# Kernel tuning notes

Hardware: AMD Instinct MI355X
Metric: run time of the kernel (lower is better)

The kernel has to match this reference:

```python
import jax, jax.numpy as jnp
import numpy as np

NA = 3          # anchors per head
NC = 3          # classes (labels < 3 are valid)
IGNORE_THRES = 0.5
OBJ_SCALE = 5.0
NOOBJ_SCALE = 0.5
GRIDS = [19, 38, 76]
SCALED_ANCHORS = [
    jnp.array([[116., 90.], [156., 198.], [373., 326.]], jnp.float32) / 32.0,  # large head
    jnp.array([[30., 61.], [62., 45.], [59., 119.]], jnp.float32) / 16.0,      # medium head
    jnp.array([[10., 13.], [16., 30.], [33., 23.]], jnp.float32) / 8.0,        # small head
]


def _safe_log(p):
    # torch BCELoss clamps log terms at -100
    return jnp.maximum(jnp.log(p), -100.0)


def _bce(p, t):
    return -(t * _safe_log(p) + (1.0 - t) * _safe_log(1.0 - p))


def _scale_loss(yolo_out, boxes, labels, anchors, G):
    B = yolo_out.shape[0]
    out = yolo_out.reshape(B, NA, G, G, -1)            # [B,3,G,G,8]
    aw = anchors[:, 0].reshape(1, NA, 1, 1)
    ah = anchors[:, 1].reshape(1, NA, 1, 1)
    # _change_bbox
    px = out[..., 0] - jnp.floor(out[..., 0])
    py = out[..., 1] - jnp.floor(out[..., 1])
    pw = jnp.log(out[..., 2] / aw + 1e-16)
    ph = jnp.log(out[..., 3] / ah + 1e-16)
    pconf = out[..., 4]
    pcls = out[..., 5:]                                 # [B,3,G,G,NC]
    # _yolo_targets (vectorized; boxes occupy distinct grid cells by construction)
    tb = boxes * G                                      # [B,nb,4]
    valid = labels < NC                                 # [B,nb]
    vf = valid.astype(out.dtype)
    gi = jnp.clip(tb[..., 0].astype(jnp.int32), 0, G - 1)
    gj = jnp.clip(tb[..., 1].astype(jnp.int32), 0, G - 1)
    bw, bh = tb[..., 2], tb[..., 3]                     # [B,nb]
    # anchor-wh IoU (same formula incl. 1e-16 placement as source)
    inter = jnp.minimum(anchors[:, 0], bw[..., None]) * jnp.minimum(anchors[:, 1], bh[..., None])
    union = anchors[:, 0] * anchors[:, 1] + 1e-16 + (bw * bh)[..., None] - inter
    iou = inter / union                                 # [B,nb,NA]
    best = jnp.argmax(iou, axis=-1)                     # [B,nb]
    bidx = jnp.arange(B)[:, None]                       # [B,1] -> broadcasts with [B,nb]
    obj = jnp.zeros((B, NA, G, G), out.dtype).at[bidx, best, gj, gi].max(vf)
    is_best = best[..., None] == jnp.arange(NA)         # [B,nb,NA]
    clear = valid[..., None] & ((iou > IGNORE_THRES) | is_best)
    keep = 1.0 - clear.astype(out.dtype)
    noobj = jnp.ones((B, NA, G, G), out.dtype).at[
        bidx[..., None], jnp.arange(NA), gj[..., None], gi[..., None]].min(keep)
    # tx/ty in the source are t_x - t_x.float() == 0, so targets stay zero
    twv = vf * jnp.log(bw / anchors[best, 0] + 1e-16)
    thv = vf * jnp.log(bh / anchors[best, 1] + 1e-16)
    tw = jnp.zeros((B, NA, G, G), out.dtype).at[bidx, best, gj, gi].set(twv)
    th = jnp.zeros((B, NA, G, G), out.dtype).at[bidx, best, gj, gi].set(thv)
    tcls = jnp.zeros((B, NA, G, G, NC), out.dtype).at[
        bidx, best, gj, gi, jnp.clip(labels, 0, NC - 1)].max(vf)
    tconf = obj
    # masked sum losses (reduction='sum' over masked elements)
    x_loss = jnp.sum(obj * px ** 2)
    y_loss = jnp.sum(obj * py ** 2)
    w_loss = jnp.sum(obj * (pw - tw) ** 2)
    h_loss = jnp.sum(obj * (ph - th) ** 2)
    conf_obj = jnp.sum(obj * _bce(pconf, tconf))
    conf_noobj = jnp.sum(noobj * _bce(pconf, tconf))
    cls_loss = jnp.sum(obj[..., None] * _bce(pcls, tcls))
    return (x_loss + y_loss + w_loss + h_loss
            + OBJ_SCALE * conf_obj + NOOBJ_SCALE * conf_noobj + cls_loss)


def reference(out_large, out_medium, out_small, boxes, labels):
    B = out_large.shape[0]
    loss = 0.0
    for out, anc, g in zip((out_large, out_medium, out_small), SCALED_ANCHORS, GRIDS):
        loss = loss + _scale_loss(out, boxes, labels, anc, g)
    return loss / B


def setup_inputs() -> dict:
    key = jax.random.key(0)
    ks = jax.random.split(key, 8)
    B, NB = 128, 12
    # predictions in (0.02, 0.98): valid BCE probs and positive w/h
    def u(k, shape):
        return 0.02 + 0.96 * jax.random.uniform(k, shape, jnp.float32)
    out_large = u(ks[0], (B, 3 * 19 * 19, 8))
    out_medium = u(ks[1], (B, 3 * 38 * 38, 8))
    out_small = u(ks[2], (B, 3 * 76 * 76, 8))
    # box centers: distinct grid columns per box at all grid sizes
    base_x = (jnp.arange(NB, dtype=jnp.float32) + 0.5) / NB
    xc = base_x[None, :] + jax.random.uniform(ks[3], (B, NB), jnp.float32, -0.004, 0.004)
    yc = jax.random.uniform(ks[4], (B, NB), jnp.float32, 0.1, 0.9)
    wh = jax.random.uniform(ks[5], (B, NB, 2), jnp.float32, 0.05, 0.4)
    boxes = jnp.concatenate([xc[..., None], yc[..., None], wh], axis=-1)
    labels = jax.random.randint(ks[6], (B, NB), 0, 5, jnp.int32)  # labels>=3 invalid
    return {"out_large": out_large, "out_medium": out_medium, "out_small": out_small,
            "boxes": boxes, "labels": labels}
```

## Files before the change

kernel.cpp:

```cpp
#include <hip/hip_runtime.h>

#define NA 3
#define NCLS 3
#define NB 12
#define BATCH 128

__device__ __forceinline__ float safelog(float x) {
    return fmaxf(logf(x), -100.0f);
}

__device__ __constant__ float AWc[3][3] = {{3.625f, 4.875f, 11.65625f},
                                           {1.875f, 3.875f, 3.6875f},
                                           {1.25f,  2.0f,   4.125f}};
__device__ __constant__ float AHc[3][3] = {{2.8125f, 6.1875f, 10.1875f},
                                           {3.8125f, 2.8125f, 7.4375f},
                                           {1.625f,  3.75f,   2.875f}};


template <int G, int S, int ITER>
__device__ __forceinline__ void scale_body(int b, int chunk,
                                           const float* __restrict__ outp,
                                           const float* __restrict__ boxes,
                                           const int* __restrict__ labels,
                                           int* sbox, float* red,
                                           float* __restrict__ partials, int pidx) {
    constexpr int CELLS = NA * G * G;
    const int tid = threadIdx.x;

    if (tid < NB) {
        float4 bx = ((const float4*)boxes)[b * NB + tid];
        int lab = labels[b * NB + tid];
        bool valid = lab < NCLS;

        float bw = bx.z * (float)G, bh = bx.w * (float)G;
        int gi = min(max((int)(bx.x * (float)G), 0), G - 1);
        int gj = min(max((int)(bx.y * (float)G), 0), G - 1);

        float iou[3]; int best = 0; float bi = -1.0f;
#pragma unroll
        for (int a = 0; a < 3; a++) {
            float aw = AWc[S][a], ah = AHc[S][a];
            float inter = fminf(aw, bw) * fminf(ah, bh);
            float uni = aw * ah + 1e-16f + bw * bh - inter;
            iou[a] = inter / uni;
            if (iou[a] > bi) { bi = iou[a]; best = a; }
        }
        int flags = 0;
        if (valid) {
#pragma unroll
            for (int a = 0; a < 3; a++)
                if (iou[a] > 0.5f || a == best) flags |= (1 << a);
            flags |= (1 << (4 + best));
        }
        sbox[tid * 6 + 0] = gi;
        sbox[tid * 6 + 1] = gj;
        sbox[tid * 6 + 2] = flags;
        sbox[tid * 6 + 3] = min(max(lab, 0), NCLS - 1);
        sbox[tid * 6 + 4] = __float_as_int(valid ? logf(bw / AWc[S][best] + 1e-16f) : 0.0f);
        sbox[tid * 6 + 5] = __float_as_int(valid ? logf(bh / AHc[S][best] + 1e-16f) : 0.0f);
    }
    __syncthreads();

    const float* outb = outp + (size_t)b * CELLS * 8;
    float acc = 0.0f;
    const int base = chunk * (256 * ITER);

#pragma unroll
    for (int k = 0; k < ITER; k++) {
        int c = base + k * 256 + tid;
        if (c < CELLS) {
            int a   = c / (G * G);
            int rem = c - a * (G * G);
            int gj  = rem / G;
            int gi  = rem - gj * G;

            const float4* p = (const float4*)(outb + (size_t)c * 8);
            float4 q0 = p[0];
            float4 q1 = p[1];

            float keepv = 1.0f;
            bool obj = false;
            float tw = 0.0f, th = 0.0f;
            int cls = 0;
#pragma unroll
            for (int n = 0; n < NB; n++) {
                if (sbox[n * 6 + 0] == gi && sbox[n * 6 + 1] == gj) {
                    int fl = sbox[n * 6 + 2];
                    if ((fl >> a) & 1) keepv = 0.0f;
                    if ((fl >> (4 + a)) & 1) {
                        obj = true;
                        cls = sbox[n * 6 + 3];
                        tw  = __int_as_float(sbox[n * 6 + 4]);
                        th  = __int_as_float(sbox[n * 6 + 5]);
                    }
                }
            }

            float conf = q1.x;
            float loss = -0.5f * keepv * safelog(1.0f - conf);

            if (obj) {
                float aw = AWc[S][a], ah = AHc[S][a];
                float px = q0.x - floorf(q0.x);
                float py = q0.y - floorf(q0.y);
                float pw = logf(q0.z / aw + 1e-16f);
                float ph = logf(q0.w / ah + 1e-16f);
                float dw = pw - tw, dh = ph - th;
                loss += px * px + py * py + dw * dw + dh * dh;
                loss += -5.0f * safelog(conf);
                float c0 = q1.y, c1 = q1.z, c2 = q1.w;
                loss -= (cls == 0) ? safelog(c0) : safelog(1.0f - c0);
                loss -= (cls == 1) ? safelog(c1) : safelog(1.0f - c1);
                loss -= (cls == 2) ? safelog(c2) : safelog(1.0f - c2);
            }
            acc += loss;
        }
    }

    red[tid] = acc;
    __syncthreads();
    for (int s = 128; s > 0; s >>= 1) {
        if (tid < s) red[tid] += red[tid + s];
        __syncthreads();
    }
    if (tid == 0) partials[pidx] = red[0];
}

__launch_bounds__(256)
__global__ void fused_loss(const float* __restrict__ oL,
                           const float* __restrict__ oM,
                           const float* __restrict__ oS,
                           const float* __restrict__ boxes,
                           const int* __restrict__ labels,
                           float* __restrict__ partials) {
    __shared__ int sbox[NB * 6];
    __shared__ float red[256];
    int idx = blockIdx.x;
    if (idx < 128) {
        scale_body<19, 0, 5>(idx, 0, oL, boxes, labels, sbox, red, partials, idx);
    } else if (idx < 640) {
        int r = idx - 128;
        scale_body<38, 1, 5>(r >> 2, r & 3, oM, boxes, labels, sbox, red, partials, idx);
    } else {
        int r = idx - 640;
        scale_body<76, 2, 8>(r / 9, r % 9, oS, boxes, labels, sbox, red, partials, idx);
    }
}

__global__ void final_reduce(const float* __restrict__ partials, int n,
                             float* __restrict__ out) {
    __shared__ float red[256];
    float acc = 0.0f;
    for (int i = threadIdx.x; i < n; i += 256) acc += partials[i];
    red[threadIdx.x] = acc;
    __syncthreads();
    for (int s = 128; s > 0; s >>= 1) {
        if (threadIdx.x < s) red[threadIdx.x] += red[threadIdx.x + s];
        __syncthreads();
    }
    if (threadIdx.x == 0) out[0] = red[0] * (1.0f / (float)BATCH);
}

extern "C" void kernel_launch(void* const* d_in, const int* in_sizes, int n_in,
                              void* d_out, int out_size, void* d_ws, size_t ws_size,
                              hipStream_t stream) {
    const float* oL     = (const float*)d_in[0];
    const float* oM     = (const float*)d_in[1];
    const float* oS     = (const float*)d_in[2];
    const float* boxes  = (const float*)d_in[3];
    const int*   labels = (const int*)d_in[4];

    float* partials = (float*)d_ws;

    fused_loss<<<1792, 256, 0, stream>>>(oL, oM, oS, boxes, labels, partials);
    final_reduce<<<1, 256, 0, stream>>>(partials, 1792, (float*)d_out);
}
```

Before: 25.83 us.

## Fuse final reduction via last-block atomic, skip box matching per wavefront, use fast log

Replaces the separate final_reduce launch with a last-block-done pattern: each block writes its partial, bumps an atomic counter, and the last block reduces all partials. A memset launch resets the counter. The per-cell loop over 12 boxes now runs only when a wavefront's cell range could hold a box cell, with packed box keys held in registers via readfirstlane. The q0 load happens only for object cells, and logf becomes __logf. This trades a kernel launch and most per-cell comparisons and loads for an atomic, a memset, and slightly less accurate logs.

```diff
diff --git a/kernel.cpp b/kernel.cpp
--- a/kernel.cpp
+++ b/kernel.cpp
@@ -4,10 +4,7 @@
 #define NCLS 3
 #define NB 12
 #define BATCH 128
-
-__device__ __forceinline__ float safelog(float x) {
-    return fmaxf(logf(x), -100.0f);
-}
+#define UNITS 1792
 
 __device__ __constant__ float AWc[3][3] = {{3.625f, 4.875f, 11.65625f},
                                            {1.875f, 3.875f, 3.6875f},
@@ -16,15 +13,20 @@
                                            {3.8125f, 2.8125f, 7.4375f},
                                            {1.625f,  3.75f,   2.875f}};
 
+__device__ __forceinline__ float safelog(float x) {
+    return fmaxf(__logf(x), -100.0f);
+}
+
 
 template <int G, int S, int ITER>
-__device__ __forceinline__ void scale_body(int b, int chunk,
-                                           const float* __restrict__ outp,
-                                           const float* __restrict__ boxes,
-                                           const int* __restrict__ labels,
-                                           int* sbox, float* red,
-                                           float* __restrict__ partials, int pidx) {
-    constexpr int CELLS = NA * G * G;
+__device__ __forceinline__ float scale_body(int b, int chunk,
+        const float* __restrict__ outp,
+        const float* __restrict__ boxes,
+        const int* __restrict__ labels,
+        int* skey, float* sdat)
+{
+    constexpr int GG = G * G;
+    constexpr int CELLS = NA * GG;
     const int tid = threadIdx.x;
 
     if (tid < NB) {
@@ -52,14 +54,16 @@
                 if (iou[a] > 0.5f || a == best) flags |= (1 << a);
             flags |= (1 << (4 + best));
         }
-        sbox[tid * 6 + 0] = gi;
-        sbox[tid * 6 + 1] = gj;
-        sbox[tid * 6 + 2] = flags;
-        sbox[tid * 6 + 3] = min(max(lab, 0), NCLS - 1);
-        sbox[tid * 6 + 4] = __float_as_int(valid ? logf(bw / AWc[S][best] + 1e-16f) : 0.0f);
-        sbox[tid * 6 + 5] = __float_as_int(valid ? logf(bh / AHc[S][best] + 1e-16f) : 0.0f);
+        int cls = min(max(lab, 0), NCLS - 1);
+        skey[tid] = (gj * G + gi) | (flags << 16) | (cls << 24);
+        sdat[tid]      = valid ? __logf(bw / AWc[S][best] + 1e-16f) : 0.0f;
+        sdat[NB + tid] = valid ? __logf(bh / AHc[S][best] + 1e-16f) : 0.0f;
     }
     __syncthreads();
+
+    int rk[NB];
+#pragma unroll
+    for (int n = 0; n < NB; n++) rk[n] = __builtin_amdgcn_readfirstlane(skey[n]);
 
     const float* outb = outp + (size_t)b * CELLS * 8;
     float acc = 0.0f;
@@ -69,42 +73,47 @@
     for (int k = 0; k < ITER; k++) {
         int c = base + k * 256 + tid;
         if (c < CELLS) {
-            int a   = c / (G * G);
-            int rem = c - a * (G * G);
-            int gj  = rem / G;
-            int gi  = rem - gj * G;
-
-            const float4* p = (const float4*)(outb + (size_t)c * 8);
-            float4 q0 = p[0];
-            float4 q1 = p[1];
+            const float* cp = outb + (size_t)c * 8;
+            float4 q1 = *(const float4*)(cp + 4);
+            float conf = q1.x;
+
+            int cw = __builtin_amdgcn_readfirstlane(c) & ~63;
+            int aw = cw / GG;
+            int r0 = cw - aw * GG;
+            bool maybe = (r0 + 63 >= GG);
+#pragma unroll
+            for (int n = 0; n < NB; n++)
+                maybe = maybe || ((unsigned)((rk[n] & 0xFFFF) - r0) < 64u);
 
             float keepv = 1.0f;
-            bool obj = false;
-            float tw = 0.0f, th = 0.0f;
-            int cls = 0;
-#pragma unroll
-            for (int n = 0; n < NB; n++) {
-                if (sbox[n * 6 + 0] == gi && sbox[n * 6 + 1] == gj) {
-                    int fl = sbox[n * 6 + 2];
-                    if ((fl >> a) & 1) keepv = 0.0f;
-                    if ((fl >> (4 + a)) & 1) {
-                        obj = true;
-                        cls = sbox[n * 6 + 3];
-                        tw  = __int_as_float(sbox[n * 6 + 4]);
-                        th  = __int_as_float(sbox[n * 6 + 5]);
+            int objn = -1;
+            int a = 0;
+            if (maybe) {
+                a = c / GG;
+                int rem = c - a * GG;
+#pragma unroll
+                for (int n = 0; n < NB; n++) {
+                    int pk = rk[n];
+                    if ((pk & 0xFFFF) == rem) {
+                        int fl = pk >> 16;
+                        if ((fl >> a) & 1) keepv = 0.0f;
+                        if ((fl >> (4 + a)) & 1) objn = n;
                     }
                 }
             }
 
-            float conf = q1.x;
             float loss = -0.5f * keepv * safelog(1.0f - conf);
 
-            if (obj) {
-                float aw = AWc[S][a], ah = AHc[S][a];
+            if (objn >= 0) {
+                float4 q0 = *(const float4*)cp;
+                int pk = rk[objn];
+                int cls = (pk >> 24) & 3;
+                float tw = sdat[objn], th = sdat[NB + objn];
+                float aws = AWc[S][a], ahs = AHc[S][a];
                 float px = q0.x - floorf(q0.x);
                 float py = q0.y - floorf(q0.y);
-                float pw = logf(q0.z / aw + 1e-16f);
-                float ph = logf(q0.w / ah + 1e-16f);
+                float pw = __logf(q0.z / aws + 1e-16f);
+                float ph = __logf(q0.w / ahs + 1e-16f);
                 float dw = pw - tw, dh = ph - th;
                 loss += px * px + py * py + dw * dw + dh * dh;
                 loss += -5.0f * safelog(conf);
@@ -116,14 +125,7 @@
             acc += loss;
         }
     }
-
-    red[tid] = acc;
-    __syncthreads();
-    for (int s = 128; s > 0; s >>= 1) {
-        if (tid < s) red[tid] += red[tid + s];
-        __syncthreads();
-    }
-    if (tid == 0) partials[pidx] = red[0];
+    return acc;
 }
 
 __launch_bounds__(256)
@@ -132,33 +134,58 @@
                            const float* __restrict__ oS,
                            const float* __restrict__ boxes,
                            const int* __restrict__ labels,
-                           float* __restrict__ partials) {
-    __shared__ int sbox[NB * 6];
+                           float* __restrict__ partials,
+                           unsigned int* __restrict__ counter,
+                           float* __restrict__ out)
+{
+    __shared__ int skey[NB];
+    __shared__ float sdat[2 * NB];
     __shared__ float red[256];
-    int idx = blockIdx.x;
-    if (idx < 128) {
-        scale_body<19, 0, 5>(idx, 0, oL, boxes, labels, sbox, red, partials, idx);
-    } else if (idx < 640) {
-        int r = idx - 128;
-        scale_body<38, 1, 5>(r >> 2, r & 3, oM, boxes, labels, sbox, red, partials, idx);
+    __shared__ int isLast;
+
+    const int u = blockIdx.x;
+    const int tid = threadIdx.x;
+
+    float acc;
+    if (u < 128) {
+        acc = scale_body<19, 0, 5>(u, 0, oL, boxes, labels, skey, sdat);
+    } else if (u < 640) {
+        int r = u - 128;
+        acc = scale_body<38, 1, 5>(r >> 2, r & 3, oM, boxes, labels, skey, sdat);
     } else {
-        int r = idx - 640;
-        scale_body<76, 2, 8>(r / 9, r % 9, oS, boxes, labels, sbox, red, partials, idx);
-    }
-}
-
-__global__ void final_reduce(const float* __restrict__ partials, int n,
-                             float* __restrict__ out) {
-    __shared__ float red[256];
-    float acc = 0.0f;
-    for (int i = threadIdx.x; i < n; i += 256) acc += partials[i];
-    red[threadIdx.x] = acc;
+        int r = u - 640;
+        acc = scale_body<76, 2, 8>(r / 9, r % 9, oS, boxes, labels, skey, sdat);
+    }
+
+    red[tid] = acc;
     __syncthreads();
+#pragma unroll
     for (int s = 128; s > 0; s >>= 1) {
-        if (threadIdx.x < s) red[threadIdx.x] += red[threadIdx.x + s];
+        if (tid < s) red[tid] += red[tid + s];
         __syncthreads();
     }
-    if (threadIdx.x == 0) out[0] = red[0] * (1.0f / (float)BATCH);
+
+    if (tid == 0) {
+        partials[u] = red[0];
+        __threadfence();
+        isLast = (atomicAdd(counter, 1u) == UNITS - 1);
+    }
+    __syncthreads();
+
+    if (isLast) {
+        __threadfence();
+        float a2 = 0.0f;
+#pragma unroll
+        for (int i = 0; i < 7; i++) a2 += partials[tid + i * 256];
+        red[tid] = a2;
+        __syncthreads();
+#pragma unroll
+        for (int s = 128; s > 0; s >>= 1) {
+            if (tid < s) red[tid] += red[tid + s];
+            __syncthreads();
+        }
+        if (tid == 0) out[0] = red[0] * (1.0f / (float)BATCH);
+    }
 }
 
 extern "C" void kernel_launch(void* const* d_in, const int* in_sizes, int n_in,
@@ -170,8 +197,10 @@
     const float* boxes  = (const float*)d_in[3];
     const int*   labels = (const int*)d_in[4];
 
-    float* partials = (float*)d_ws;
-
-    fused_loss<<<1792, 256, 0, stream>>>(oL, oM, oS, boxes, labels, partials);
-    final_reduce<<<1, 256, 0, stream>>>(partials, 1792, (float*)d_out);
-}
+    float* partials   = (float*)d_ws;
+    unsigned* counter = (unsigned*)((char*)d_ws + UNITS * sizeof(float));
+
+    hipMemsetAsync(counter, 0, sizeof(unsigned), stream);
+    fused_loss<<<UNITS, 256, 0, stream>>>(oL, oM, oS, boxes, labels,
+                                          partials, counter, (float*)d_out);
+}
```

After: 75.34 us. +191.7%, slower.
